# Kernel tuning notes

Hardware: AMD Instinct MI355X
Metric: run time of the kernel (lower is better)

## Reference

```python
import jax, jax.numpy as jnp
import numpy as np

N_NODES = 100000
N_EDGES = 1600000
IN_F, HID_F, OUT_F = 128, 128, 64


def gcn_conv(x, edge_index, W, b):
    # x: [N, Fin]; W: [Fout, Fin] (torch Linear layout); b: [Fout]
    h = x @ W.T + b  # [N, Fout]
    src, dst = edge_index[0], edge_index[1]
    n = x.shape[0]
    # in-degree via scatter-add of ones on dst (matches torch code)
    deg = jax.ops.segment_sum(jnp.ones(src.shape[0], dtype=h.dtype), dst, num_segments=n)
    deg_inv_sqrt = jnp.where(deg > 0, deg ** -0.5, 0.0)
    w = deg_inv_sqrt[src] * deg_inv_sqrt[dst]  # edge_weight defaults to ones
    msg = w[:, None] * h[src]  # [E, Fout] gather + scale
    return jax.ops.segment_sum(msg, dst, num_segments=n)  # scatter-add aggregate


def setup_inputs() -> dict:
    key = jax.random.key(0)
    k1, k2, k3, k4 = jax.random.split(key, 4)
    x = jax.random.normal(k1, (N_NODES, IN_F), dtype=jnp.float32)
    edge_index = jax.random.randint(k2, (2, N_EDGES), 0, N_NODES, dtype=jnp.int64)
    # xavier-uniform-like weights, zero bias (torch Linear layout [out, in])
    lim1 = float(np.sqrt(6.0 / (IN_F + HID_F)))
    lim2 = float(np.sqrt(6.0 / (HID_F + OUT_F)))
    W1 = jax.random.uniform(k3, (HID_F, IN_F), jnp.float32, -lim1, lim1)
    W2 = jax.random.uniform(k4, (OUT_F, HID_F), jnp.float32, -lim2, lim2)
    b1 = jnp.zeros((HID_F,), jnp.float32)
    b2 = jnp.zeros((OUT_F,), jnp.float32)
    return {"x": x, "edge_index": edge_index, "W1": W1, "b1": b1, "W2": W2, "b2": b2}


def reference(x, edge_index, W1, b1, W2, b2):
    # layer 1 + relu (dropout is identity in eval mode)
    h = jax.nn.relu(gcn_conv(x, edge_index, W1, b1))
    # final layer, no activation
    return gcn_conv(h, edge_index, W2, b2)
```

## Files before the change

### kernel.cpp

```cpp
#include <hip/hip_runtime.h>

constexpr int FIN    = 128;
constexpr int LOG_RB = 7;
constexpr int RB     = 1 << LOG_RB;
constexpr int BMAX   = 1024;
constexpr int CAP    = 4096;
constexpr int CHUNK  = 4096;
constexpr int EPT    = CHUNK / 256;

typedef _Float16 half8 __attribute__((ext_vector_type(8)));
typedef float    f32x4 __attribute__((ext_vector_type(4)));

__global__ __launch_bounds__(1024) void init_gcur_kernel(int* __restrict__ gcur, int B) {
    int i = blockIdx.x * 1024 + threadIdx.x;
    if (i < B) gcur[i] = i * CAP;
}

__global__ __launch_bounds__(256) void bucket_scatter_kernel(
    const int* __restrict__ src, const int* __restrict__ dst,
    int* __restrict__ gcur, unsigned* __restrict__ gEdges, int E, int B)
{
    __shared__ int lhist[BMAX];
    __shared__ int lbase[BMAX];
    const int e0 = blockIdx.x * CHUNK;
    const int e1 = min(e0 + CHUNK, E);
    for (int i = threadIdx.x; i < B; i += 256) lhist[i] = 0;
    __syncthreads();

    int dreg[EPT];
    int rank[EPT];
    #pragma unroll
    for (int k = 0; k < EPT; ++k) {
        int e = e0 + k * 256 + threadIdx.x;
        dreg[k] = (e < e1) ? dst[e] : -1;
        rank[k] = (dreg[k] >= 0) ? atomicAdd(&lhist[dreg[k] >> LOG_RB], 1) : 0;
    }
    __syncthreads();
    for (int i = threadIdx.x; i < B; i += 256) {
        int c = lhist[i];
        if (c) lbase[i] = atomicAdd(&gcur[i], c);
    }
    __syncthreads();
    #pragma unroll
    for (int k = 0; k < EPT; ++k) {
        if (dreg[k] >= 0) {
            int e = e0 + k * 256 + threadIdx.x;
            int b = dreg[k] >> LOG_RB;
            int pos = lbase[b] + rank[k];
            if (pos < (b + 1) * CAP)
                gEdges[pos] = ((unsigned)src[e] << LOG_RB) | (unsigned)(dreg[k] & (RB - 1));
        }
    }
}

__global__ __launch_bounds__(256) void finalize_kernel(
    const unsigned* __restrict__ gEdges, const int* __restrict__ gcur,
    int* __restrict__ rbeg, int* __restrict__ rend, float* __restrict__ dis,
    int* __restrict__ esrc, int N)
{
    __shared__ int h[RB];
    __shared__ int excl[RB];
    __shared__ unsigned sedge[CAP];
    __shared__ short    srank[CAP];
    const int b = blockIdx.x;
    const int base = b * CAP;
    int cnt = gcur[b] - base;
    if (cnt > CAP) cnt = CAP;
    const int node0 = b << LOG_RB;
    if (threadIdx.x < RB) h[threadIdx.x] = 0;
    __syncthreads();
    for (int i = threadIdx.x; i < cnt; i += 256) {
        unsigned p = gEdges[base + i];
        sedge[i] = p;
        srank[i] = (short)atomicAdd(&h[p & (RB - 1)], 1);
    }
    __syncthreads();
    if (threadIdx.x < RB) excl[threadIdx.x] = h[threadIdx.x];
    __syncthreads();
    for (int off = 1; off < RB; off <<= 1) {
        int u = 0;
        if (threadIdx.x < RB && threadIdx.x >= off) u = excl[threadIdx.x - off];
        __syncthreads();
        if (threadIdx.x < RB) excl[threadIdx.x] += u;
        __syncthreads();
    }
    if (threadIdx.x < RB) {
        int c  = h[threadIdx.x];
        int ex = excl[threadIdx.x] - c;
        int node = node0 + threadIdx.x;
        if (node < N) {
            rbeg[node] = base + ex;
            rend[node] = base + ex + c;
            dis[node]  = c > 0 ? rsqrtf((float)c) : 0.0f;
        }
        excl[threadIdx.x] = ex;
    }
    __syncthreads();
    for (int i = threadIdx.x; i < cnt; i += 256) {
        unsigned p = sedge[i];
        int dl = (int)(p & (RB - 1));
        esrc[base + excl[dl] + (int)srank[i]] = (int)(p >> LOG_RB);
    }
}

__global__ __launch_bounds__(256) void linear1_kernel(
    const float* __restrict__ X, const float* __restrict__ W,
    const float* __restrict__ Bv, const float* __restrict__ dis,
    _Float16* __restrict__ Y, int N)
{
    __shared__ __align__(16) _Float16 xs[64 * 128];
    const int tid  = threadIdx.x;
    const int wave = tid >> 6;
    const int lane = tid & 63;
    const int l15  = lane & 15;
    const int lhi  = lane >> 4;

    half8 wf[2][4];
    float bias[2];
    #pragma unroll
    for (int c = 0; c < 2; ++c) {
        int f = (wave * 2 + c) * 16 + l15;
        #pragma unroll
        for (int ks = 0; ks < 4; ++ks) {
            const float* wp = &W[f * 128 + ks * 32 + lhi * 8];
            float4 u0 = *(const float4*)wp;
            float4 u1 = *(const float4*)(wp + 4);
            half8 hh;
            hh[0] = (_Float16)u0.x; hh[1] = (_Float16)u0.y;
            hh[2] = (_Float16)u0.z; hh[3] = (_Float16)u0.w;
            hh[4] = (_Float16)u1.x; hh[5] = (_Float16)u1.y;
            hh[6] = (_Float16)u1.z; hh[7] = (_Float16)u1.w;
            wf[c][ks] = hh;
        }
        bias[c] = Bv[f];
    }

    const int nchunks = (N + 63) / 64;
    for (int ch = blockIdx.x; ch < nchunks; ch += gridDim.x) {
        const int n0 = ch * 64;
        __syncthreads();
        #pragma unroll
        for (int p = 0; p < 4; ++p) {
            int ci  = p * 256 + tid;
            int row = ci >> 4, c = ci & 15;
            int n   = n0 + row;
            int nc  = n < N ? n : N - 1;
            const float* xp = &X[(size_t)nc * 128 + c * 8];
            float4 u0 = *(const float4*)xp;
            float4 u1 = *(const float4*)(xp + 4);
            half8 hh;
            hh[0] = (_Float16)u0.x; hh[1] = (_Float16)u0.y;
            hh[2] = (_Float16)u0.z; hh[3] = (_Float16)u0.w;
            hh[4] = (_Float16)u1.x; hh[5] = (_Float16)u1.y;
            hh[6] = (_Float16)u1.z; hh[7] = (_Float16)u1.w;
            *(half8*)&xs[row * 128 + (c ^ (row & 7)) * 8] = hh;
        }
        __syncthreads();

        f32x4 acc[4][2];
        #pragma unroll
        for (int mt = 0; mt < 4; ++mt)
            #pragma unroll
            for (int c = 0; c < 2; ++c) {
                acc[mt][c][0] = bias[c]; acc[mt][c][1] = bias[c];
                acc[mt][c][2] = bias[c]; acc[mt][c][3] = bias[c];
            }

        #pragma unroll
        for (int mt = 0; mt < 4; ++mt) {
            int row = mt * 16 + l15;
            #pragma unroll
            for (int ks = 0; ks < 4; ++ks) {
                int c  = ks * 4 + lhi;
                half8 a = *(const half8*)&xs[row * 128 + (c ^ (row & 7)) * 8];
                #pragma unroll
                for (int c2 = 0; c2 < 2; ++c2)
                    acc[mt][c2] = __builtin_amdgcn_mfma_f32_16x16x32_f16(
                        a, wf[c2][ks], acc[mt][c2], 0, 0, 0);
            }
        }
        __syncthreads();
        #pragma unroll
        for (int mt = 0; mt < 4; ++mt)
            #pragma unroll
            for (int r = 0; r < 4; ++r) {
                int row = mt * 16 + lhi * 4 + r;
                int n   = n0 + row;
                int nc  = n < N ? n : N - 1;
                float dv = dis[nc];
                #pragma unroll
                for (int c2 = 0; c2 < 2; ++c2) {
                    int col = (wave * 2 + c2) * 16 + l15;
                    xs[row * 128 + col] = (_Float16)(dv * acc[mt][c2][r]);
                }
            }
        __syncthreads();
        #pragma unroll
        for (int p = 0; p < 4; ++p) {
            int ci  = p * 256 + tid;
            int row = ci >> 4, c = ci & 15;
            int n   = n0 + row;
            if (n < N)
                *(half8*)&Y[(size_t)n * 128 + c * 8] = *(const half8*)&xs[row * 128 + c * 8];
        }
    }
}

__global__ __launch_bounds__(256) void aggregate128h_kernel(
    const _Float16* __restrict__ H, const int* __restrict__ rbeg,
    const int* __restrict__ rend, const int* __restrict__ esrc,
    const float* __restrict__ dis, _Float16* __restrict__ OUT, int N)
{
    const int lane = threadIdx.x & 15;
    const int d = blockIdx.x * 16 + (threadIdx.x >> 4);
    if (d >= N) return;
    const int beg = rbeg[d], end = rend[d];
    float acc[4][8];
    #pragma unroll
    for (int u = 0; u < 4; ++u)
        #pragma unroll
        for (int j = 0; j < 8; ++j) acc[u][j] = 0.0f;

    const int n4 = (end - beg) >> 2;
    int e = beg;
    if (n4 > 0) {
        int s0 = esrc[e], s1 = esrc[e+1], s2 = esrc[e+2], s3 = esrc[e+3];
        for (int q = 1; q < n4; ++q) {
            const int b2 = beg + q * 4;
            int t0 = esrc[b2], t1 = esrc[b2+1], t2 = esrc[b2+2], t3 = esrc[b2+3];
            half8 v0 = *(const half8*)&H[(size_t)s0 * 128 + lane * 8];
            half8 v1 = *(const half8*)&H[(size_t)s1 * 128 + lane * 8];
            half8 v2 = *(const half8*)&H[(size_t)s2 * 128 + lane * 8];
            half8 v3 = *(const half8*)&H[(size_t)s3 * 128 + lane * 8];
            #pragma unroll
            for (int j = 0; j < 8; ++j) {
                acc[0][j] += (float)v0[j]; acc[1][j] += (float)v1[j];
                acc[2][j] += (float)v2[j]; acc[3][j] += (float)v3[j];
            }
            s0 = t0; s1 = t1; s2 = t2; s3 = t3;
        }
        {
            half8 v0 = *(const half8*)&H[(size_t)s0 * 128 + lane * 8];
            half8 v1 = *(const half8*)&H[(size_t)s1 * 128 + lane * 8];
            half8 v2 = *(const half8*)&H[(size_t)s2 * 128 + lane * 8];
            half8 v3 = *(const half8*)&H[(size_t)s3 * 128 + lane * 8];
            #pragma unroll
            for (int j = 0; j < 8; ++j) {
                acc[0][j] += (float)v0[j]; acc[1][j] += (float)v1[j];
                acc[2][j] += (float)v2[j]; acc[3][j] += (float)v3[j];
            }
        }
        e = beg + n4 * 4;
    }
    for (; e < end; ++e) {
        int s0 = esrc[e];
        half8 v0 = *(const half8*)&H[(size_t)s0 * 128 + lane * 8];
        #pragma unroll
        for (int j = 0; j < 8; ++j) acc[0][j] += (float)v0[j];
    }
    float w = dis[d];
    half8 o;
    #pragma unroll
    for (int j = 0; j < 8; ++j) {
        float t = w * ((acc[0][j] + acc[1][j]) + (acc[2][j] + acc[3][j]));
        o[j] = (_Float16)fmaxf(t, 0.0f);
    }
    *(half8*)&OUT[(size_t)d * 128 + lane * 8] = o;
}

__global__ __launch_bounds__(256) void lin2_kernel(
    const _Float16* __restrict__ Xh, const float* __restrict__ W,
    const float* __restrict__ Bv, const float* __restrict__ dis,
    _Float16* __restrict__ Y, int N)
{
    __shared__ __align__(16) _Float16 xs[64 * 128];
    const int tid  = threadIdx.x;
    const int wave = tid >> 6;
    const int lane = tid & 63;
    const int l15  = lane & 15;
    const int lhi  = lane >> 4;

    half8 wf[4];
    float bias;
    {
        int f = wave * 16 + l15;
        #pragma unroll
        for (int ks = 0; ks < 4; ++ks) {
            const float* wp = &W[f * 128 + ks * 32 + lhi * 8];
            float4 u0 = *(const float4*)wp;
            float4 u1 = *(const float4*)(wp + 4);
            half8 hh;
            hh[0] = (_Float16)u0.x; hh[1] = (_Float16)u0.y;
            hh[2] = (_Float16)u0.z; hh[3] = (_Float16)u0.w;
            hh[4] = (_Float16)u1.x; hh[5] = (_Float16)u1.y;
            hh[6] = (_Float16)u1.z; hh[7] = (_Float16)u1.w;
            wf[ks] = hh;
        }
        bias = Bv[f];
    }

    const int nchunks = (N + 63) / 64;
    for (int ch = blockIdx.x; ch < nchunks; ch += gridDim.x) {
        const int n0 = ch * 64;
        __syncthreads();
        #pragma unroll
        for (int p = 0; p < 4; ++p) {
            int ci  = p * 256 + tid;
            int row = ci >> 4, c = ci & 15;
            int n   = n0 + row;
            int nc  = n < N ? n : N - 1;
            half8 hh = *(const half8*)&Xh[(size_t)nc * 128 + c * 8];
            *(half8*)&xs[row * 128 + (c ^ (row & 7)) * 8] = hh;
        }
        __syncthreads();

        f32x4 acc[4];
        #pragma unroll
        for (int mt = 0; mt < 4; ++mt) {
            acc[mt][0] = bias; acc[mt][1] = bias;
            acc[mt][2] = bias; acc[mt][3] = bias;
        }
        #pragma unroll
        for (int mt = 0; mt < 4; ++mt) {
            int row = mt * 16 + l15;
            #pragma unroll
            for (int ks = 0; ks < 4; ++ks) {
                int c  = ks * 4 + lhi;
                half8 a = *(const half8*)&xs[row * 128 + (c ^ (row & 7)) * 8];
                acc[mt] = __builtin_amdgcn_mfma_f32_16x16x32_f16(a, wf[ks], acc[mt], 0, 0, 0);
            }
        }
        __syncthreads();
        #pragma unroll
        for (int mt = 0; mt < 4; ++mt)
            #pragma unroll
            for (int r = 0; r < 4; ++r) {
                int row = mt * 16 + lhi * 4 + r;
                int n   = n0 + row;
                int nc  = n < N ? n : N - 1;
                float dv = dis[nc];
                xs[row * 64 + wave * 16 + l15] = (_Float16)(dv * acc[mt][r]);
            }
        __syncthreads();
        #pragma unroll
        for (int p = 0; p < 2; ++p) {
            int ci  = p * 256 + tid;
            int row = ci >> 3, c = ci & 7;
            int n   = n0 + row;
            if (n < N)
                *(half8*)&Y[(size_t)n * 64 + c * 8] = *(const half8*)&xs[row * 64 + c * 8];
        }
    }
}

__global__ __launch_bounds__(256) void aggregate64h_kernel(
    const _Float16* __restrict__ H, const int* __restrict__ rbeg,
    const int* __restrict__ rend, const int* __restrict__ esrc,
    const float* __restrict__ dis, float* __restrict__ OUT, int N)
{
    const int lane = threadIdx.x & 7;
    const int d = blockIdx.x * 32 + (threadIdx.x >> 3);
    if (d >= N) return;
    const int beg = rbeg[d], end = rend[d];
    float acc[4][8];
    #pragma unroll
    for (int u = 0; u < 4; ++u)
        #pragma unroll
        for (int j = 0; j < 8; ++j) acc[u][j] = 0.0f;

    const int n4 = (end - beg) >> 2;
    int e = beg;
    if (n4 > 0) {
        int s0 = esrc[e], s1 = esrc[e+1], s2 = esrc[e+2], s3 = esrc[e+3];
        for (int q = 1; q < n4; ++q) {
            const int b2 = beg + q * 4;
            int t0 = esrc[b2], t1 = esrc[b2+1], t2 = esrc[b2+2], t3 = esrc[b2+3];
            half8 v0 = *(const half8*)&H[(size_t)s0 * 64 + lane * 8];
            half8 v1 = *(const half8*)&H[(size_t)s1 * 64 + lane * 8];
            half8 v2 = *(const half8*)&H[(size_t)s2 * 64 + lane * 8];
            half8 v3 = *(const half8*)&H[(size_t)s3 * 64 + lane * 8];
            #pragma unroll
            for (int j = 0; j < 8; ++j) {
                acc[0][j] += (float)v0[j]; acc[1][j] += (float)v1[j];
                acc[2][j] += (float)v2[j]; acc[3][j] += (float)v3[j];
            }
            s0 = t0; s1 = t1; s2 = t2; s3 = t3;
        }
        {
            half8 v0 = *(const half8*)&H[(size_t)s0 * 64 + lane * 8];
            half8 v1 = *(const half8*)&H[(size_t)s1 * 64 + lane * 8];
            half8 v2 = *(const half8*)&H[(size_t)s2 * 64 + lane * 8];
            half8 v3 = *(const half8*)&H[(size_t)s3 * 64 + lane * 8];
            #pragma unroll
            for (int j = 0; j < 8; ++j) {
                acc[0][j] += (float)v0[j]; acc[1][j] += (float)v1[j];
                acc[2][j] += (float)v2[j]; acc[3][j] += (float)v3[j];
            }
        }
        e = beg + n4 * 4;
    }
    for (; e < end; ++e) {
        int s0 = esrc[e];
        half8 v0 = *(const half8*)&H[(size_t)s0 * 64 + lane * 8];
        #pragma unroll
        for (int j = 0; j < 8; ++j) acc[0][j] += (float)v0[j];
    }
    float w = dis[d];
    float4 o0, o1;
    o0.x = w * ((acc[0][0] + acc[1][0]) + (acc[2][0] + acc[3][0]));
    o0.y = w * ((acc[0][1] + acc[1][1]) + (acc[2][1] + acc[3][1]));
    o0.z = w * ((acc[0][2] + acc[1][2]) + (acc[2][2] + acc[3][2]));
    o0.w = w * ((acc[0][3] + acc[1][3]) + (acc[2][3] + acc[3][3]));
    o1.x = w * ((acc[0][4] + acc[1][4]) + (acc[2][4] + acc[3][4]));
    o1.y = w * ((acc[0][5] + acc[1][5]) + (acc[2][5] + acc[3][5]));
    o1.z = w * ((acc[0][6] + acc[1][6]) + (acc[2][6] + acc[3][6]));
    o1.w = w * ((acc[0][7] + acc[1][7]) + (acc[2][7] + acc[3][7]));
    float* p = &OUT[(size_t)d * 64 + lane * 8];
    *(float4*)p = o0;
    *(float4*)(p + 4) = o1;
}

template <int FOUT, bool RELU_IN>
__global__ __launch_bounds__(256) void linear_kernel(
    const float* __restrict__ X, const float* __restrict__ W,
    const float* __restrict__ Bv, float* __restrict__ Y, int N)
{
    constexpr int TX = FOUT / 4;
    constexpr int TY = 256 / TX;
    constexpr int NB = 4 * TY;
    constexpr int QMASK = TX - 1;
    __shared__ float ws[FIN * FOUT];
    __shared__ float xs[NB * FIN];
    const int tid = threadIdx.x;
    const int tx  = tid % TX;
    const int ty  = tid / TX;
    for (int i = tid; i < FOUT * FIN; i += 256) {
        int f = i >> 7;
        int k = i & (FIN - 1);
        int q = f >> 2, r = f & 3;
        int qq = q ^ (k & QMASK);
        ws[k * FOUT + qq * 4 + r] = W[i];
    }
    const float4 bv = *(const float4*)&Bv[tx * 4];
    const int nchunks = (N + NB - 1) / NB;
    for (int c = blockIdx.x; c < nchunks; c += gridDim.x) {
        const int n0 = c * NB;
        __syncthreads();
        constexpr int V4 = FIN / 4;
        for (int i4 = tid; i4 < NB * V4; i4 += 256) {
            int row = i4 / V4, c4 = i4 % V4;
            int n = n0 + row;
            int nc = n < N ? n : N - 1;
            float4 v = *(const float4*)&X[(long long)nc * FIN + c4 * 4];
            if (RELU_IN) {
                v.x = fmaxf(v.x, 0.0f); v.y = fmaxf(v.y, 0.0f);
                v.z = fmaxf(v.z, 0.0f); v.w = fmaxf(v.w, 0.0f);
            }
            *(float4*)&xs[row * FIN + c4 * 4] = v;
        }
        __syncthreads();
        float acc[4][4];
        #pragma unroll
        for (int j = 0; j < 4; ++j) {
            acc[j][0] = bv.x; acc[j][1] = bv.y; acc[j][2] = bv.z; acc[j][3] = bv.w;
        }
        #pragma unroll 2
        for (int k = 0; k < FIN; k += 4) {
            float w[4][4];
            #pragma unroll
            for (int kk = 0; kk < 4; ++kk) {
                int kr = k + kk;
                float4 t = *(const float4*)&ws[kr * FOUT + ((tx ^ (kr & QMASK)) << 2)];
                w[kk][0] = t.x; w[kk][1] = t.y; w[kk][2] = t.z; w[kk][3] = t.w;
            }
            float xr[4][4];
            #pragma unroll
            for (int j = 0; j < 4; ++j) {
                float4 t = *(const float4*)&xs[(ty * 4 + j) * FIN + k];
                xr[j][0] = t.x; xr[j][1] = t.y; xr[j][2] = t.z; xr[j][3] = t.w;
            }
            #pragma unroll
            for (int j = 0; j < 4; ++j)
                #pragma unroll
                for (int kk = 0; kk < 4; ++kk) {
                    acc[j][0] = fmaf(xr[j][kk], w[kk][0], acc[j][0]);
                    acc[j][1] = fmaf(xr[j][kk], w[kk][1], acc[j][1]);
                    acc[j][2] = fmaf(xr[j][kk], w[kk][2], acc[j][2]);
                    acc[j][3] = fmaf(xr[j][kk], w[kk][3], acc[j][3]);
                }
        }
        #pragma unroll
        for (int j = 0; j < 4; ++j) {
            int n = n0 + ty * 4 + j;
            if (n < N) {
                float4 o;
                o.x = acc[j][0]; o.y = acc[j][1]; o.z = acc[j][2]; o.w = acc[j][3];
                *(float4*)&Y[(long long)n * FOUT + tx * 4] = o;
            }
        }
    }
}

template <int LOGF>
__global__ __launch_bounds__(256) void scatter_kernel(
    const float* __restrict__ H, const int* __restrict__ src,
    const int* __restrict__ dst, const float* __restrict__ dis,
    float* __restrict__ OUT, int E)
{
    constexpr int F = 1 << LOGF;
    const long long total  = (long long)E << LOGF;
    const long long stride = (long long)gridDim.x * blockDim.x;
    for (long long i = (long long)blockIdx.x * blockDim.x + threadIdx.x;
         i < total; i += stride) {
        int e = (int)(i >> LOGF);
        int f = (int)i & (F - 1);
        int s = src[e];
        int d = dst[e];
        float w = dis[s] * dis[d];
        atomicAdd(&OUT[d * F + f], w * H[s * F + f]);
    }
}

__global__ __launch_bounds__(256) void dis_inplace_kernel(float* __restrict__ deg, int N) {
    int i = blockIdx.x * 256 + threadIdx.x;
    if (i < N) {
        float d = deg[i];
        deg[i] = d > 0.0f ? rsqrtf(d) : 0.0f;
    }
}

__global__ __launch_bounds__(256) void deg_kernel_f(const int* __restrict__ dst,
                                                    float* __restrict__ deg, int E) {
    int stride = gridDim.x * 256;
    for (int i = blockIdx.x * 256 + threadIdx.x; i < E; i += stride)
        atomicAdd(&deg[dst[i]], 1.0f);
}

static inline size_t align512(size_t x) { return (x + 511) & ~(size_t)511; }

extern "C" void kernel_launch(void* const* d_in, const int* in_sizes, int n_in,
                              void* d_out, int out_size, void* d_ws, size_t ws_size,
                              hipStream_t stream)
{
    const float* x  = (const float*)d_in[0];
    const int*   ei = (const int*)d_in[1];
    const float* W1 = (const float*)d_in[2];
    const float* b1 = (const float*)d_in[3];
    const float* W2 = (const float*)d_in[4];
    const float* b2 = (const float*)d_in[5];

    const int N = in_sizes[0] / FIN;
    const int E = in_sizes[1] / 2;
    const int* src = ei;
    const int* dst = ei + E;
    float* out = (float*)d_out;
    char* wsb = (char*)d_ws;

    const int B = (N + RB - 1) / RB;

    size_t hreg = (size_t)N * 128 * 2;
    size_t areg = (size_t)B * CAP * 4;
    size_t h1sz = hreg > areg ? hreg : areg;
    size_t o = 0;
    int*      gcur  = (int*)(wsb + o);      o = align512(o + (size_t)BMAX * 4);
    int*      rbeg  = (int*)(wsb + o);      o = align512(o + (size_t)N * 4);
    int*      rendp = (int*)(wsb + o);      o = align512(o + (size_t)N * 4);
    float*    dis   = (float*)(wsb + o);    o = align512(o + (size_t)N * 4);
    int*      esrcA = (int*)(wsb + o);      o = align512(o + areg);
    _Float16* h1    = (_Float16*)(wsb + o); o = align512(o + h1sz);
    _Float16* agg1  = (_Float16*)(wsb + o); o = align512(o + (size_t)N * 128 * 2);
    _Float16* h2    = (_Float16*)(wsb + o); o = align512(o + (size_t)N * 64 * 2);
    size_t need = o;
    unsigned* gEdges = (unsigned*)h1;

    if (ws_size >= need && B <= BMAX) {
        init_gcur_kernel<<<(B + 1023) / 1024, 1024, 0, stream>>>(gcur, B);
        bucket_scatter_kernel<<<(E + CHUNK - 1) / CHUNK, 256, 0, stream>>>(
            src, dst, gcur, gEdges, E, B);
        finalize_kernel<<<B, 256, 0, stream>>>(gEdges, gcur, rbeg, rendp, dis, esrcA, N);

        linear1_kernel<<<512, 256, 0, stream>>>(x, W1, b1, dis, h1, N);
        aggregate128h_kernel<<<(N + 15) / 16, 256, 0, stream>>>(h1, rbeg, rendp,
                                                                esrcA, dis, agg1, N);
        lin2_kernel<<<512, 256, 0, stream>>>(agg1, W2, b2, dis, h2, N);
        aggregate64h_kernel<<<(N + 31) / 32, 256, 0, stream>>>(h2, rbeg, rendp,
                                                               esrcA, dis, out, N);
    } else {
        float* deg  = (float*)wsb;
        size_t off  = align512((size_t)N * 4);
        float* fh1  = (float*)(wsb + off);
        float* fagg = fh1 + (size_t)N * FIN;
        float* fh2  = fh1;

        hipMemsetAsync(deg,  0, (size_t)N * 4, stream);
        hipMemsetAsync(fagg, 0, (size_t)N * FIN * 4, stream);
        hipMemsetAsync(out,  0, (size_t)N * 64 * 4, stream);

        deg_kernel_f<<<2048, 256, 0, stream>>>(dst, deg, E);
        dis_inplace_kernel<<<(N + 255) / 256, 256, 0, stream>>>(deg, N);

        linear_kernel<128, false><<<512, 256, 0, stream>>>(x, W1, b1, fh1, N);
        scatter_kernel<7><<<8192, 256, 0, stream>>>(fh1, src, dst, deg, fagg, E);
        linear_kernel<64, true><<<512, 256, 0, stream>>>(fagg, W2, b2, fh2, N);
        scatter_kernel<6><<<8192, 256, 0, stream>>>(fh2, src, dst, deg, out, E);
    }
}
```

Measured before the change: 173.8 us.

## Store node features in 16-column feature slices to localize gathers per aggregation block

The intermediate feature tensors change from row-major [N, F] to a sliced layout [F/16][N][16]. The linear kernels now write and read this layout, and the aggregation kernels assign each block to one slice with two threads per node. The goal is a per-slice gather working set (N×16 halves, about 3.2 MB) small enough to stay in L2 or MALL, which should cut misses on random neighbor gathers. In exchange, each block re-reads the CSR indices and rbeg/rend once per slice (8x for layer 1), and each gather fetches only 32 contiguous bytes per node.

```diff
diff --git a/kernel.cpp b/kernel.cpp
--- a/kernel.cpp
+++ b/kernel.cpp
@@ -106,7 +106,7 @@
 __global__ __launch_bounds__(256) void linear1_kernel(
     const float* __restrict__ X, const float* __restrict__ W,
     const float* __restrict__ Bv, const float* __restrict__ dis,
-    _Float16* __restrict__ Y, int N)
+    _Float16* __restrict__ Ys, int N)
 {
     __shared__ __align__(16) _Float16 xs[64 * 128];
     const int tid  = threadIdx.x;
@@ -197,23 +197,30 @@
         __syncthreads();
         #pragma unroll
         for (int p = 0; p < 4; ++p) {
-            int ci  = p * 256 + tid;
-            int row = ci >> 4, c = ci & 15;
-            int n   = n0 + row;
+            int id  = p * 256 + tid;
+            int s   = id >> 7;
+            int r   = (id >> 1) & 63;
+            int sub = id & 1;
+            int n   = n0 + r;
             if (n < N)
-                *(half8*)&Y[(size_t)n * 128 + c * 8] = *(const half8*)&xs[row * 128 + c * 8];
-        }
-    }
-}
-
-__global__ __launch_bounds__(256) void aggregate128h_kernel(
-    const _Float16* __restrict__ H, const int* __restrict__ rbeg,
+                *(half8*)&Ys[(((size_t)s * N) + n) * 16 + sub * 8] =
+                    *(const half8*)&xs[r * 128 + s * 16 + sub * 8];
+        }
+    }
+}
+
+__global__ __launch_bounds__(256) void aggregate128s_kernel(
+    const _Float16* __restrict__ Hs, const int* __restrict__ rbeg,
     const int* __restrict__ rend, const int* __restrict__ esrc,
-    const float* __restrict__ dis, _Float16* __restrict__ OUT, int N)
-{
-    const int lane = threadIdx.x & 15;
-    const int d = blockIdx.x * 16 + (threadIdx.x >> 4);
+    const float* __restrict__ dis, _Float16* __restrict__ OUTs, int N)
+{
+    const int slice = blockIdx.x & 7;
+    const int grp   = blockIdx.x >> 3;
+    const int d     = grp * 128 + (threadIdx.x >> 1);
+    const int sub   = threadIdx.x & 1;
     if (d >= N) return;
+    const _Float16* H = Hs + (size_t)slice * N * 16 + sub * 8;
+
     const int beg = rbeg[d], end = rend[d];
     float acc[4][8];
     #pragma unroll
@@ -228,10 +235,10 @@
         for (int q = 1; q < n4; ++q) {
             const int b2 = beg + q * 4;
             int t0 = esrc[b2], t1 = esrc[b2+1], t2 = esrc[b2+2], t3 = esrc[b2+3];
-            half8 v0 = *(const half8*)&H[(size_t)s0 * 128 + lane * 8];
-            half8 v1 = *(const half8*)&H[(size_t)s1 * 128 + lane * 8];
-            half8 v2 = *(const half8*)&H[(size_t)s2 * 128 + lane * 8];
-            half8 v3 = *(const half8*)&H[(size_t)s3 * 128 + lane * 8];
+            half8 v0 = *(const half8*)&H[(size_t)s0 * 16];
+            half8 v1 = *(const half8*)&H[(size_t)s1 * 16];
+            half8 v2 = *(const half8*)&H[(size_t)s2 * 16];
+            half8 v3 = *(const half8*)&H[(size_t)s3 * 16];
             #pragma unroll
             for (int j = 0; j < 8; ++j) {
                 acc[0][j] += (float)v0[j]; acc[1][j] += (float)v1[j];
@@ -240,10 +247,10 @@
             s0 = t0; s1 = t1; s2 = t2; s3 = t3;
         }
         {
-            half8 v0 = *(const half8*)&H[(size_t)s0 * 128 + lane * 8];
-            half8 v1 = *(const half8*)&H[(size_t)s1 * 128 + lane * 8];
-            half8 v2 = *(const half8*)&H[(size_t)s2 * 128 + lane * 8];
-            half8 v3 = *(const half8*)&H[(size_t)s3 * 128 + lane * 8];
+            half8 v0 = *(const half8*)&H[(size_t)s0 * 16];
+            half8 v1 = *(const half8*)&H[(size_t)s1 * 16];
+            half8 v2 = *(const half8*)&H[(size_t)s2 * 16];
+            half8 v3 = *(const half8*)&H[(size_t)s3 * 16];
             #pragma unroll
             for (int j = 0; j < 8; ++j) {
                 acc[0][j] += (float)v0[j]; acc[1][j] += (float)v1[j];
@@ -254,7 +261,7 @@
     }
     for (; e < end; ++e) {
         int s0 = esrc[e];
-        half8 v0 = *(const half8*)&H[(size_t)s0 * 128 + lane * 8];
+        half8 v0 = *(const half8*)&H[(size_t)s0 * 16];
         #pragma unroll
         for (int j = 0; j < 8; ++j) acc[0][j] += (float)v0[j];
     }
@@ -265,13 +272,13 @@
         float t = w * ((acc[0][j] + acc[1][j]) + (acc[2][j] + acc[3][j]));
         o[j] = (_Float16)fmaxf(t, 0.0f);
     }
-    *(half8*)&OUT[(size_t)d * 128 + lane * 8] = o;
+    *(half8*)&OUTs[(((size_t)slice * N) + d) * 16 + sub * 8] = o;
 }
 
 __global__ __launch_bounds__(256) void lin2_kernel(
-    const _Float16* __restrict__ Xh, const float* __restrict__ W,
+    const _Float16* __restrict__ Xs, const float* __restrict__ W,
     const float* __restrict__ Bv, const float* __restrict__ dis,
-    _Float16* __restrict__ Y, int N)
+    _Float16* __restrict__ Ys, int N)
 {
     __shared__ __align__(16) _Float16 xs[64 * 128];
     const int tid  = threadIdx.x;
@@ -305,12 +312,15 @@
         __syncthreads();
         #pragma unroll
         for (int p = 0; p < 4; ++p) {
-            int ci  = p * 256 + tid;
-            int row = ci >> 4, c = ci & 15;
-            int n   = n0 + row;
+            int id  = p * 256 + tid;
+            int s   = id >> 7;
+            int r   = (id >> 1) & 63;
+            int sub = id & 1;
+            int n   = n0 + r;
             int nc  = n < N ? n : N - 1;
-            half8 hh = *(const half8*)&Xh[(size_t)nc * 128 + c * 8];
-            *(half8*)&xs[row * 128 + (c ^ (row & 7)) * 8] = hh;
+            half8 hh = *(const half8*)&Xs[(((size_t)s * N) + nc) * 16 + sub * 8];
+            int c = s * 2 + sub;
+            *(half8*)&xs[r * 128 + (c ^ (r & 7)) * 8] = hh;
         }
         __syncthreads();
 
@@ -344,23 +354,31 @@
         __syncthreads();
         #pragma unroll
         for (int p = 0; p < 2; ++p) {
-            int ci  = p * 256 + tid;
-            int row = ci >> 3, c = ci & 7;
-            int n   = n0 + row;
+            int id  = p * 256 + tid;
+            int s   = id >> 7;
+            int r   = (id >> 1) & 63;
+            int sub = id & 1;
+            int n   = n0 + r;
             if (n < N)
-                *(half8*)&Y[(size_t)n * 64 + c * 8] = *(const half8*)&xs[row * 64 + c * 8];
-        }
-    }
-}
-
-__global__ __launch_bounds__(256) void aggregate64h_kernel(
-    const _Float16* __restrict__ H, const int* __restrict__ rbeg,
+                *(half8*)&Ys[(((size_t)s * N) + n) * 16 + sub * 8] =
+                    *(const half8*)&xs[r * 64 + s * 16 + sub * 8];
+        }
+    }
+}
+
+__global__ __launch_bounds__(256) void aggregate64s_kernel(
+    const _Float16* __restrict__ Hs, const int* __restrict__ rbeg,
     const int* __restrict__ rend, const int* __restrict__ esrc,
     const float* __restrict__ dis, float* __restrict__ OUT, int N)
 {
-    const int lane = threadIdx.x & 7;
-    const int d = blockIdx.x * 32 + (threadIdx.x >> 3);
+    const int q     = blockIdx.x & 7;
+    const int slice = q >> 1;
+    const int half  = q & 1;
+    const int d     = (blockIdx.x >> 3) * 256 + half * 128 + (threadIdx.x >> 1);
+    const int sub   = threadIdx.x & 1;
     if (d >= N) return;
+    const _Float16* H = Hs + (size_t)slice * N * 16 + sub * 8;
+
     const int beg = rbeg[d], end = rend[d];
     float acc[4][8];
     #pragma unroll
@@ -372,13 +390,13 @@
     int e = beg;
     if (n4 > 0) {
         int s0 = esrc[e], s1 = esrc[e+1], s2 = esrc[e+2], s3 = esrc[e+3];
-        for (int q = 1; q < n4; ++q) {
-            const int b2 = beg + q * 4;
+        for (int qq = 1; qq < n4; ++qq) {
+            const int b2 = beg + qq * 4;
             int t0 = esrc[b2], t1 = esrc[b2+1], t2 = esrc[b2+2], t3 = esrc[b2+3];
-            half8 v0 = *(const half8*)&H[(size_t)s0 * 64 + lane * 8];
-            half8 v1 = *(const half8*)&H[(size_t)s1 * 64 + lane * 8];
-            half8 v2 = *(const half8*)&H[(size_t)s2 * 64 + lane * 8];
-            half8 v3 = *(const half8*)&H[(size_t)s3 * 64 + lane * 8];
+            half8 v0 = *(const half8*)&H[(size_t)s0 * 16];
+            half8 v1 = *(const half8*)&H[(size_t)s1 * 16];
+            half8 v2 = *(const half8*)&H[(size_t)s2 * 16];
+            half8 v3 = *(const half8*)&H[(size_t)s3 * 16];
             #pragma unroll
             for (int j = 0; j < 8; ++j) {
                 acc[0][j] += (float)v0[j]; acc[1][j] += (float)v1[j];
@@ -387,10 +405,10 @@
             s0 = t0; s1 = t1; s2 = t2; s3 = t3;
         }
         {
-            half8 v0 = *(const half8*)&H[(size_t)s0 * 64 + lane * 8];
-            half8 v1 = *(const half8*)&H[(size_t)s1 * 64 + lane * 8];
-            half8 v2 = *(const half8*)&H[(size_t)s2 * 64 + lane * 8];
-            half8 v3 = *(const half8*)&H[(size_t)s3 * 64 + lane * 8];
+            half8 v0 = *(const half8*)&H[(size_t)s0 * 16];
+            half8 v1 = *(const half8*)&H[(size_t)s1 * 16];
+            half8 v2 = *(const half8*)&H[(size_t)s2 * 16];
+            half8 v3 = *(const half8*)&H[(size_t)s3 * 16];
             #pragma unroll
             for (int j = 0; j < 8; ++j) {
                 acc[0][j] += (float)v0[j]; acc[1][j] += (float)v1[j];
@@ -401,7 +419,7 @@
     }
     for (; e < end; ++e) {
         int s0 = esrc[e];
-        half8 v0 = *(const half8*)&H[(size_t)s0 * 64 + lane * 8];
+        half8 v0 = *(const half8*)&H[(size_t)s0 * 16];
         #pragma unroll
         for (int j = 0; j < 8; ++j) acc[0][j] += (float)v0[j];
     }
@@ -415,7 +433,7 @@
     o1.y = w * ((acc[0][5] + acc[1][5]) + (acc[2][5] + acc[3][5]));
     o1.z = w * ((acc[0][6] + acc[1][6]) + (acc[2][6] + acc[3][6]));
     o1.w = w * ((acc[0][7] + acc[1][7]) + (acc[2][7] + acc[3][7]));
-    float* p = &OUT[(size_t)d * 64 + lane * 8];
+    float* p = &OUT[(size_t)d * 64 + slice * 16 + sub * 8];
     *(float4*)p = o0;
     *(float4*)(p + 4) = o1;
 }
@@ -567,11 +585,11 @@
     int*      rendp = (int*)(wsb + o);      o = align512(o + (size_t)N * 4);
     float*    dis   = (float*)(wsb + o);    o = align512(o + (size_t)N * 4);
     int*      esrcA = (int*)(wsb + o);      o = align512(o + areg);
-    _Float16* h1    = (_Float16*)(wsb + o); o = align512(o + h1sz);
-    _Float16* agg1  = (_Float16*)(wsb + o); o = align512(o + (size_t)N * 128 * 2);
-    _Float16* h2    = (_Float16*)(wsb + o); o = align512(o + (size_t)N * 64 * 2);
+    _Float16* h1s   = (_Float16*)(wsb + o); o = align512(o + h1sz);
+    _Float16* agg1s = (_Float16*)(wsb + o); o = align512(o + (size_t)N * 128 * 2);
+    _Float16* h2s   = (_Float16*)(wsb + o); o = align512(o + (size_t)N * 64 * 2);
     size_t need = o;
-    unsigned* gEdges = (unsigned*)h1;
+    unsigned* gEdges = (unsigned*)h1s;
 
     if (ws_size >= need && B <= BMAX) {
         init_gcur_kernel<<<(B + 1023) / 1024, 1024, 0, stream>>>(gcur, B);
@@ -579,12 +597,12 @@
             src, dst, gcur, gEdges, E, B);
         finalize_kernel<<<B, 256, 0, stream>>>(gEdges, gcur, rbeg, rendp, dis, esrcA, N);
 
-        linear1_kernel<<<512, 256, 0, stream>>>(x, W1, b1, dis, h1, N);
-        aggregate128h_kernel<<<(N + 15) / 16, 256, 0, stream>>>(h1, rbeg, rendp,
-                                                                esrcA, dis, agg1, N);
-        lin2_kernel<<<512, 256, 0, stream>>>(agg1, W2, b2, dis, h2, N);
-        aggregate64h_kernel<<<(N + 31) / 32, 256, 0, stream>>>(h2, rbeg, rendp,
-                                                               esrcA, dis, out, N);
+        linear1_kernel<<<512, 256, 0, stream>>>(x, W1, b1, dis, h1s, N);
+        aggregate128s_kernel<<<((N + 127) / 128) * 8, 256, 0, stream>>>(
+            h1s, rbeg, rendp, esrcA, dis, agg1s, N);
+        lin2_kernel<<<512, 256, 0, stream>>>(agg1s, W2, b2, dis, h2s, N);
+        aggregate64s_kernel<<<((N + 255) / 256) * 8, 256, 0, stream>>>(
+            h2s, rbeg, rendp, esrcA, dis, out, N);
     } else {
         float* deg  = (float*)wsb;
         size_t off  = align512((size_t)N * 4);
```

Result: slower. 208.7 us (+20.1%).
